# Kernel optimization log

Measured on AMD Instinct MI355X. Metric: run time of the kernel, lower is better.

Reference implementation:

```python
import jax, jax.numpy as jnp
import numpy as np
from jax.ops import segment_sum

NUM_NODES = 100000
HIDDEN = 128
NUM_LAYERS = 3
EDGES = 640000
BN_EPS = 1e-5


def setup_inputs() -> dict:
    key = jax.random.key(0)
    ks = jax.random.split(key, 6)
    edge_index = jax.random.randint(ks[0], (2, EDGES), 0, NUM_NODES, dtype=jnp.int32)
    # xavier-ish init for embedding (hidden-1 dims; last dim is log-degree feature)
    emb_weight = jax.random.normal(ks[1], (NUM_NODES, HIDDEN - 1), dtype=jnp.float32) * 0.02
    # GCNConv linear weights [L, in, out] and biases [L, out]
    Ws = jax.random.normal(ks[2], (NUM_LAYERS, HIDDEN, HIDDEN), dtype=jnp.float32) * (1.0 / np.sqrt(HIDDEN))
    bs = jnp.zeros((NUM_LAYERS, HIDDEN), dtype=jnp.float32)
    gammas = jnp.ones((NUM_LAYERS, HIDDEN), dtype=jnp.float32)
    betas = jnp.zeros((NUM_LAYERS, HIDDEN), dtype=jnp.float32)
    return {"emb_weight": emb_weight, "Ws": Ws, "bs": bs,
            "gammas": gammas, "betas": betas, "edge_index": edge_index}


def reference(emb_weight, Ws, bs, gammas, betas, edge_index):
    row, col = edge_index[0], edge_index[1]  # source, target
    N = emb_weight.shape[0]
    ones_e = jnp.ones(row.shape[0], dtype=emb_weight.dtype)

    # node_degree_features = log(out_degree + 1) (degree of edge_index[0])
    deg_src = segment_sum(ones_e, row, num_segments=N)
    x = jnp.concatenate([emb_weight, jnp.log(deg_src + 1.0)[:, None]], axis=1)  # [N, H]

    # GCN symmetric normalization (add_self_loops=False): deg over targets
    deg = segment_sum(ones_e, col, num_segments=N)
    dinv = jnp.where(deg > 0, jax.lax.rsqrt(jnp.maximum(deg, 1.0)), 0.0)
    norm = dinv[row] * dinv[col]  # [E]

    for i in range(Ws.shape[0]):
        x_prev = x
        h = x @ Ws[i]  # [N, H]
        # scatter-add of normalized messages: out[col] += norm * h[row]
        agg = segment_sum(norm[:, None] * h[row], col, num_segments=N) + bs[i]
        # BatchNorm1d (batch statistics, biased variance)
        mean = agg.mean(axis=0)
        var = agg.var(axis=0)
        x = gammas[i] * (agg - mean) * jax.lax.rsqrt(var + BN_EPS) + betas[i]
        x = jax.nn.relu(x)
        if i > 0:
            x = x + 0.5 * x_prev
    return x
```

## Files before the change

### kernel.cpp

```cpp
#include <hip/hip_runtime.h>
#include <hip/hip_bf16.h>
#include <math.h>

#define BN_EPS 1e-5f

typedef __attribute__((ext_vector_type(8))) short short8v;
typedef __attribute__((ext_vector_type(4))) float f32x4;
typedef __attribute__((ext_vector_type(2))) int int2v;
typedef __attribute__((ext_vector_type(4))) unsigned int uint4v;
typedef __attribute__((ext_vector_type(4))) float float4v;

__device__ inline float bf_lo(unsigned int p) { return __uint_as_float(p << 16); }
__device__ inline float bf_hi(unsigned int p) { return __uint_as_float(p & 0xffff0000u); }
__device__ inline unsigned int packbf(float a, float b) {
    unsigned short lo = __builtin_bit_cast(unsigned short, __float2bfloat16(a));
    unsigned short hi = __builtin_bit_cast(unsigned short, __float2bfloat16(b));
    return (unsigned int)lo | ((unsigned int)hi << 16);
}


__global__ __launch_bounds__(256) void deg_kernel(const int* __restrict__ row, const int* __restrict__ col,
                                                  float* __restrict__ deg_src, float* __restrict__ deg_dst, int E) {
    int e = blockIdx.x * 256 + threadIdx.x;
    if (e < E) {
        atomicAdd(&deg_src[row[e]], 1.0f);
        atomicAdd(&deg_dst[col[e]], 1.0f);
    }
}

__global__ __launch_bounds__(256) void dinv_cnt_kernel(float* __restrict__ deg_dst, int* __restrict__ cnt, int N) {
    int n = blockIdx.x * 256 + threadIdx.x;
    if (n < N) {
        float d = deg_dst[n];
        cnt[n] = (int)d;
        deg_dst[n] = (d > 0.0f) ? rsqrtf(d) : 0.0f;
    }
}

__global__ __launch_bounds__(256) void initx_kernel(const float* __restrict__ emb, const float* __restrict__ deg_src,
                                                    unsigned int* __restrict__ x, int N) {
    int idx = blockIdx.x * 256 + threadIdx.x;
    if (idx < N * 64) {
        int n = idx >> 6, p = idx & 63;
        float v0, v1;
        if (p < 63) {
            v0 = emb[(size_t)n * 127 + 2 * p];
            v1 = emb[(size_t)n * 127 + 2 * p + 1];
        } else {
            v0 = emb[(size_t)n * 127 + 126];
            v1 = logf(deg_src[n] + 1.0f);
        }
        x[idx] = packbf(v0, v1);
    }
}

__global__ __launch_bounds__(256) void wt_kernel(const float* __restrict__ Ws, __hip_bfloat16* __restrict__ Wt) {
    int idx = blockIdx.x * 256 + threadIdx.x;
    if (idx < 3 * 16384) {
        int l = idx >> 14, rem = idx & 16383, c = rem >> 7, k = rem & 127;
        Wt[idx] = __float2bfloat16(Ws[(l << 14) + (k << 7) + c]);
    }
}


__global__ __launch_bounds__(256) void scan_pass1(const int* __restrict__ cnt, int* __restrict__ blockSums,
                                                  int N, int PT) {
    __shared__ int lds[256];
    const int tid = threadIdx.x;
    const int start = (blockIdx.x * 256 + tid) * PT;
    int s = 0;
    for (int i = 0; i < PT; ++i) {
        int idx = start + i;
        if (idx < N) s += cnt[idx];
    }
    lds[tid] = s;
    __syncthreads();
    for (int d = 128; d > 0; d >>= 1) {
        if (tid < d) lds[tid] += lds[tid + d];
        __syncthreads();
    }
    if (tid == 0) blockSums[blockIdx.x] = lds[0];
}

__global__ __launch_bounds__(256) void scan_pass2(const int* __restrict__ blockSums, int* __restrict__ blockOffs) {
    __shared__ int lds[256];
    const int tid = threadIdx.x;
    int v = blockSums[tid];
    lds[tid] = v;
    __syncthreads();
    for (int d = 1; d < 256; d <<= 1) {
        int t = (tid >= d) ? lds[tid - d] : 0;
        __syncthreads();
        lds[tid] += t;
        __syncthreads();
    }
    blockOffs[tid] = lds[tid] - v;
}

__global__ __launch_bounds__(256) void scan_pass3(const int* __restrict__ cnt, const int* __restrict__ blockOffs,
                                                  int* __restrict__ off, int* __restrict__ cur,
                                                  int N, int PT, int E) {
    __shared__ int lds[256];
    const int tid = threadIdx.x;
    const int start = (blockIdx.x * 256 + tid) * PT;
    int s = 0;
    for (int i = 0; i < PT; ++i) {
        int idx = start + i;
        if (idx < N) s += cnt[idx];
    }
    lds[tid] = s;
    __syncthreads();
    for (int d = 1; d < 256; d <<= 1) {
        int t = (tid >= d) ? lds[tid - d] : 0;
        __syncthreads();
        lds[tid] += t;
        __syncthreads();
    }
    int prefix = blockOffs[blockIdx.x] + lds[tid] - s;
    for (int i = 0; i < PT; ++i) {
        int idx = start + i;
        if (idx < N) {
            off[idx] = prefix;
            cur[idx] = prefix;
            prefix += cnt[idx];
        }
    }
    if (blockIdx.x == 0 && tid == 0) off[N] = E;
}

__global__ __launch_bounds__(256) void fill_kernel(const int* __restrict__ row, const int* __restrict__ col,
                                                   const float* __restrict__ dinv, int* __restrict__ cur,
                                                   int2* __restrict__ meta, int E) {
    int e = blockIdx.x * 256 + threadIdx.x;
    if (e < E) {
        int r = row[e], t = col[e];
        int p = atomicAdd(&cur[t], 1);
        meta[p] = make_int2(r, __float_as_int(dinv[r] * dinv[t]));
    }
}


__global__ __launch_bounds__(256) void gemm_mfma(const __hip_bfloat16* __restrict__ X,
                                                 const __hip_bfloat16* __restrict__ Wt,
                                                 __hip_bfloat16* __restrict__ H, float* __restrict__ sums,
                                                 int nStripes, int N) {
    if (blockIdx.x == 0) sums[threadIdx.x] = 0.0f;

    const int lane = threadIdx.x & 63;
    const int wv = threadIdx.x >> 6;
    const int r = lane & 15;
    const int q = lane >> 4;
    const int ch = (blockIdx.x * 4 + wv) & 1;

    short8v bfrag[4][4];
#pragma unroll
    for (int ct = 0; ct < 4; ++ct)
#pragma unroll
        for (int kk = 0; kk < 4; ++kk)
            bfrag[ct][kk] = *(const short8v*)(Wt + ((ch * 64 + ct * 16 + r) << 7) + kk * 32 + q * 8);

    const int totalJobs = nStripes * 2;
    for (int job = blockIdx.x * 4 + wv; job < totalJobs; job += gridDim.x * 4) {
        const int s = job >> 1;
        const int arow = s * 16 + r;
        short8v a0 = {}, a1 = {}, a2 = {}, a3 = {};
        if (arow < N) {
            const __hip_bfloat16* xp = X + ((size_t)arow << 7) + q * 8;
            a0 = *(const short8v*)(xp);
            a1 = *(const short8v*)(xp + 32);
            a2 = *(const short8v*)(xp + 64);
            a3 = *(const short8v*)(xp + 96);
        }
        f32x4 acc[4];
#pragma unroll
        for (int ct = 0; ct < 4; ++ct) {
            f32x4 c = {0.f, 0.f, 0.f, 0.f};
            c = __builtin_amdgcn_mfma_f32_16x16x32_bf16(a0, bfrag[ct][0], c, 0, 0, 0);
            c = __builtin_amdgcn_mfma_f32_16x16x32_bf16(a1, bfrag[ct][1], c, 0, 0, 0);
            c = __builtin_amdgcn_mfma_f32_16x16x32_bf16(a2, bfrag[ct][2], c, 0, 0, 0);
            c = __builtin_amdgcn_mfma_f32_16x16x32_bf16(a3, bfrag[ct][3], c, 0, 0, 0);
            acc[ct] = c;
        }
#pragma unroll
        for (int g = 0; g < 4; ++g) {
            int grow = s * 16 + q * 4 + g;
            if (grow < N) {
                __hip_bfloat16* hp = H + ((size_t)grow << 7) + ch * 64 + r;
#pragma unroll
                for (int ct = 0; ct < 4; ++ct)
                    hp[ct * 16] = __float2bfloat16(acc[ct][g]);
            }
        }
    }
}


__global__ __launch_bounds__(256) void gather_kernel(const __hip_bfloat16* __restrict__ h,
                                                     const int* __restrict__ off, const int2* __restrict__ meta,
                                                     const float* __restrict__ bias,
                                                     unsigned int* __restrict__ aggb, float* __restrict__ sums, int N) {
    __shared__ float sm[2][4][128];
    const int tid = threadIdx.x;
    const int lane = tid & 63;
    const int w = tid >> 6;
    const int g = lane >> 4;
    const int s = lane & 15;

    float b8[8];
    *(float4*)&b8[0] = *(const float4*)&bias[s * 8];
    *(float4*)&b8[4] = *(const float4*)&bias[s * 8 + 4];

    float psum[8], psq[8];
#pragma unroll
    for (int j = 0; j < 8; ++j) { psum[j] = 0.f; psq[j] = 0.f; }

    for (int base = (blockIdx.x * 4 + w) * 2; base < N; base += gridDim.x * 8) {
        const int nA = __builtin_amdgcn_readfirstlane(base);
        const int hasB = (nA + 1 < N);
        const int sA = off[nA];
        const int eA = off[nA + 1];
        const int eB = hasB ? off[nA + 2] : eA;

        float accA[8], accB[8];
#pragma unroll
        for (int j = 0; j < 8; ++j) { accA[j] = 0.f; accB[j] = 0.f; }

        int iA = sA, iB = eA;
        while (iA < eA || iB < eB) {
            int i0A = iA + g, i1A = iA + 4 + g;
            int i0B = iB + g, i1B = iB + 4 + g;
            int idx0A = (i0A < eA) ? i0A : 0;
            int idx1A = (i1A < eA) ? i1A : 0;
            int idx0B = (i0B < eB) ? i0B : 0;
            int idx1B = (i1B < eB) ? i1B : 0;
            int2v m0A = __builtin_nontemporal_load((const int2v*)&meta[idx0A]);
            int2v m1A = __builtin_nontemporal_load((const int2v*)&meta[idx1A]);
            int2v m0B = __builtin_nontemporal_load((const int2v*)&meta[idx0B]);
            int2v m1B = __builtin_nontemporal_load((const int2v*)&meta[idx1B]);
            float w0A = (i0A < eA) ? __int_as_float(m0A[1]) : 0.f;
            float w1A = (i1A < eA) ? __int_as_float(m1A[1]) : 0.f;
            float w0B = (i0B < eB) ? __int_as_float(m0B[1]) : 0.f;
            float w1B = (i1B < eB) ? __int_as_float(m1B[1]) : 0.f;
            short8v h0A = *(const short8v*)(h + ((size_t)m0A[0] << 7) + s * 8);
            short8v h1A = *(const short8v*)(h + ((size_t)m1A[0] << 7) + s * 8);
            short8v h0B = *(const short8v*)(h + ((size_t)m0B[0] << 7) + s * 8);
            short8v h1B = *(const short8v*)(h + ((size_t)m1B[0] << 7) + s * 8);
#pragma unroll
            for (int j = 0; j < 4; ++j) {
                unsigned int u;
                u = ((const unsigned int*)&h0A)[j];
                accA[2 * j]     = fmaf(w0A, bf_lo(u), accA[2 * j]);
                accA[2 * j + 1] = fmaf(w0A, bf_hi(u), accA[2 * j + 1]);
                u = ((const unsigned int*)&h1A)[j];
                accA[2 * j]     = fmaf(w1A, bf_lo(u), accA[2 * j]);
                accA[2 * j + 1] = fmaf(w1A, bf_hi(u), accA[2 * j + 1]);
                u = ((const unsigned int*)&h0B)[j];
                accB[2 * j]     = fmaf(w0B, bf_lo(u), accB[2 * j]);
                accB[2 * j + 1] = fmaf(w0B, bf_hi(u), accB[2 * j + 1]);
                u = ((const unsigned int*)&h1B)[j];
                accB[2 * j]     = fmaf(w1B, bf_lo(u), accB[2 * j]);
                accB[2 * j + 1] = fmaf(w1B, bf_hi(u), accB[2 * j + 1]);
            }
            iA += 8; iB += 8;
        }
#pragma unroll
        for (int j = 0; j < 8; ++j) {
            accA[j] += __shfl_xor(accA[j], 16);
            accA[j] += __shfl_xor(accA[j], 32);
            accA[j] += b8[j];
            accB[j] += __shfl_xor(accB[j], 16);
            accB[j] += __shfl_xor(accB[j], 32);
            accB[j] += b8[j];
        }
        if (g == 0) {
            uint4v pk;
#pragma unroll
            for (int j = 0; j < 4; ++j) pk[j] = packbf(accA[2 * j], accA[2 * j + 1]);
            __builtin_nontemporal_store(pk, (uint4v*)(aggb + ((size_t)nA << 6) + s * 4));
#pragma unroll
            for (int j = 0; j < 8; ++j) {
                psum[j] += accA[j];
                psq[j] = fmaf(accA[j], accA[j], psq[j]);
            }
            if (hasB) {
#pragma unroll
                for (int j = 0; j < 8; ++j) {
                    psum[j] += accB[j];
                    psq[j] = fmaf(accB[j], accB[j], psq[j]);
                }
            }
        } else if (g == 1 && hasB) {
            uint4v pk;
#pragma unroll
            for (int j = 0; j < 4; ++j) pk[j] = packbf(accB[2 * j], accB[2 * j + 1]);
            __builtin_nontemporal_store(pk, (uint4v*)(aggb + ((size_t)(nA + 1) << 6) + s * 4));
        }
    }
    if (g == 0) {
#pragma unroll
        for (int j = 0; j < 8; ++j) {
            sm[0][w][s * 8 + j] = psum[j];
            sm[1][w][s * 8 + j] = psq[j];
        }
    }
    __syncthreads();
    if (tid < 128) {
        atomicAdd(&sums[tid], sm[0][0][tid] + sm[0][1][tid] + sm[0][2][tid] + sm[0][3][tid]);
    } else {
        int c = tid - 128;
        atomicAdd(&sums[128 + c], sm[1][0][c] + sm[1][1][c] + sm[1][2][c] + sm[1][3][c]);
    }
}


template <int MODE>
__global__ __launch_bounds__(256) void bn_apply(const unsigned int* __restrict__ aggb, const float* __restrict__ sums,
                                                const float* __restrict__ gamma, const float* __restrict__ beta,
                                                const uint4* __restrict__ xprev, void* __restrict__ xout,
                                                int NO, float invN) {
    int idx = blockIdx.x * 256 + threadIdx.x;
    if (idx >= NO) return;
    const int c0 = (idx & 15) * 8;

    float su[8], sq[8], gm[8], bt[8];
    *(float4*)&su[0] = *(const float4*)&sums[c0];
    *(float4*)&su[4] = *(const float4*)&sums[c0 + 4];
    *(float4*)&sq[0] = *(const float4*)&sums[128 + c0];
    *(float4*)&sq[4] = *(const float4*)&sums[128 + c0 + 4];
    *(float4*)&gm[0] = *(const float4*)&gamma[c0];
    *(float4*)&gm[4] = *(const float4*)&gamma[c0 + 4];
    *(float4*)&bt[0] = *(const float4*)&beta[c0];
    *(float4*)&bt[4] = *(const float4*)&beta[c0 + 4];

    float sc[8], sh[8];
#pragma unroll
    for (int j = 0; j < 8; ++j) {
        float m = su[j] * invN;
        float v = sq[j] * invN - m * m;
        float inv = rsqrtf(fmaxf(v, 0.0f) + BN_EPS);
        sc[j] = gm[j] * inv;
        sh[j] = bt[j] - m * sc[j];
    }

    uint4v av = __builtin_nontemporal_load((const uint4v*)(aggb + (size_t)idx * 4));
    float r[8];
#pragma unroll
    for (int j = 0; j < 4; ++j) {
        r[2 * j]     = fmaxf(fmaf(bf_lo(av[j]), sc[2 * j],     sh[2 * j]),     0.f);
        r[2 * j + 1] = fmaxf(fmaf(bf_hi(av[j]), sc[2 * j + 1], sh[2 * j + 1]), 0.f);
    }
    if (MODE >= 1) {
        uint4 xv = xprev[idx];
        const unsigned int* xu = (const unsigned int*)&xv;
#pragma unroll
        for (int j = 0; j < 4; ++j) {
            r[2 * j]     = fmaf(0.5f, bf_lo(xu[j]), r[2 * j]);
            r[2 * j + 1] = fmaf(0.5f, bf_hi(xu[j]), r[2 * j + 1]);
        }
    }
    if (MODE == 2) {
        float* op = (float*)xout + (size_t)idx * 8;
        float4v lo = {r[0], r[1], r[2], r[3]};
        float4v hi = {r[4], r[5], r[6], r[7]};
        __builtin_nontemporal_store(lo, (float4v*)op);
        __builtin_nontemporal_store(hi, (float4v*)(op + 4));
    } else {
        unsigned int pk[4];
#pragma unroll
        for (int j = 0; j < 4; ++j) pk[j] = packbf(r[2 * j], r[2 * j + 1]);
        ((uint4*)xout)[idx] = *(uint4*)pk;
    }
}


extern "C" void kernel_launch(void* const* d_in, const int* in_sizes, int n_in,
                              void* d_out, int out_size, void* d_ws, size_t ws_size,
                              hipStream_t stream) {
    const float* emb    = (const float*)d_in[0];
    const float* Ws     = (const float*)d_in[1];
    const float* bs     = (const float*)d_in[2];
    const float* gammas = (const float*)d_in[3];
    const float* betas  = (const float*)d_in[4];
    const int*   ei     = (const int*)d_in[5];

    const int N = in_sizes[0] / 127;
    const int E = in_sizes[5] / 2;
    const int* row = ei;
    const int* col = ei + E;
    float* out = (float*)d_out;

    const size_t NH = (size_t)N * 128;
    __hip_bfloat16* XA = (__hip_bfloat16*)d_ws;
    __hip_bfloat16* XB = XA + NH;
    unsigned int*  AGG = (unsigned int*)(XB + NH);
    int2*         meta = (int2*)(AGG + NH / 2);
    __hip_bfloat16* Wt = (__hip_bfloat16*)(meta + E);
    float* deg_src = (float*)(Wt + 3 * 16384);
    float* dinvb   = deg_src + N;
    float* sums    = dinvb + N;
    int*   cnt     = (int*)(sums + 256);
    int*   cur     = cnt + N;
    int*   blockSums = cur + N;
    int*   blockOffs = blockSums + 256;
    int*   off     = blockOffs + 256;

    const int NO = (int)(NH / 8);
    const int PT = (N + 65535) / 65536;
    const int nStripes = (N + 15) / 16;
    const float invN = 1.0f / (float)N;

    hipMemsetAsync(deg_src, 0, sizeof(float) * 2 * (size_t)N, stream);
    wt_kernel<<<(3 * 16384 + 255) / 256, 256, 0, stream>>>(Ws, Wt);
    deg_kernel<<<(E + 255) / 256, 256, 0, stream>>>(row, col, deg_src, dinvb, E);
    dinv_cnt_kernel<<<(N + 255) / 256, 256, 0, stream>>>(dinvb, cnt, N);
    initx_kernel<<<(N * 64 + 255) / 256, 256, 0, stream>>>(emb, deg_src, (unsigned int*)XA, N);
    scan_pass1<<<256, 256, 0, stream>>>(cnt, blockSums, N, PT);
    scan_pass2<<<1, 256, 0, stream>>>(blockSums, blockOffs);
    scan_pass3<<<256, 256, 0, stream>>>(cnt, blockOffs, off, cur, N, PT, E);
    fill_kernel<<<(E + 255) / 256, 256, 0, stream>>>(row, col, dinvb, cur, meta, E);

    const __hip_bfloat16* xin[3]  = {XA, XA, XB};
    __hip_bfloat16*       hbuf[3] = {XB, XB, XA};

    for (int i = 0; i < 3; ++i) {
        gemm_mfma<<<1024, 256, 0, stream>>>(xin[i], Wt + (size_t)i * 16384, hbuf[i], sums, nStripes, N);
        gather_kernel<<<2048, 256, 0, stream>>>(hbuf[i], off, meta, bs + i * 128, AGG, sums, N);
        if (i == 0)
            bn_apply<0><<<(NO + 255) / 256, 256, 0, stream>>>(AGG, sums, gammas, betas,
                                                              (const uint4*)xin[i], (void*)XA, NO, invN);
        else if (i == 1)
            bn_apply<1><<<(NO + 255) / 256, 256, 0, stream>>>(AGG, sums, gammas + 128, betas + 128,
                                                              (const uint4*)xin[i], (void*)XB, NO, invN);
        else
            bn_apply<2><<<(NO + 255) / 256, 256, 0, stream>>>(AGG, sums, gammas + 256, betas + 256,
                                                              (const uint4*)xin[i], (void*)out, NO, invN);
    }
}
```

Baseline: 459.0 us.

## Fuse BatchNorm apply into next layer's MFMA GEMM prologue

BatchNorm normalization, ReLU and the residual add of layers 0 and 1 now run inside the next layer's GEMM, which builds its A fragments from the normalized values. One of the two column-half waves also writes the new activation for the later residual. This removes two standalone bn_apply launches and one round trip of the activation through memory. The cost is that the BN scale and shift are recomputed per fragment. The output buffer serves as scratch for the last H, and the BN sums now alternate between two buffers, with each fused kernel zeroing the next layer's sums.

```diff
diff --git a/kernel.cpp b/kernel.cpp
--- a/kernel.cpp
+++ b/kernel.cpp
@@ -179,6 +179,105 @@
             c = __builtin_amdgcn_mfma_f32_16x16x32_bf16(a1, bfrag[ct][1], c, 0, 0, 0);
             c = __builtin_amdgcn_mfma_f32_16x16x32_bf16(a2, bfrag[ct][2], c, 0, 0, 0);
             c = __builtin_amdgcn_mfma_f32_16x16x32_bf16(a3, bfrag[ct][3], c, 0, 0, 0);
+            acc[ct] = c;
+        }
+#pragma unroll
+        for (int g = 0; g < 4; ++g) {
+            int grow = s * 16 + q * 4 + g;
+            if (grow < N) {
+                __hip_bfloat16* hp = H + ((size_t)grow << 7) + ch * 64 + r;
+#pragma unroll
+                for (int ct = 0; ct < 4; ++ct)
+                    hp[ct * 16] = __float2bfloat16(acc[ct][g]);
+            }
+        }
+    }
+}
+
+
+template <int MODE>
+__global__ __launch_bounds__(256) void bn_gemm(const unsigned int* __restrict__ aggb, const float* __restrict__ sums,
+                                               const float* __restrict__ gamma, const float* __restrict__ beta,
+                                               const unsigned int* __restrict__ xprevb, unsigned int* __restrict__ xoutb,
+                                               const __hip_bfloat16* __restrict__ Wt, __hip_bfloat16* __restrict__ H,
+                                               float* __restrict__ sumsNext, int nStripes, int N, float invN) {
+    if (blockIdx.x == 0) sumsNext[threadIdx.x] = 0.0f;
+
+    const int lane = threadIdx.x & 63;
+    const int wv = threadIdx.x >> 6;
+    const int r = lane & 15;
+    const int q = lane >> 4;
+    const int ch = (blockIdx.x * 4 + wv) & 1;
+
+    short8v bfrag[4][4];
+#pragma unroll
+    for (int ct = 0; ct < 4; ++ct)
+#pragma unroll
+        for (int kk = 0; kk < 4; ++kk)
+            bfrag[ct][kk] = *(const short8v*)(Wt + ((ch * 64 + ct * 16 + r) << 7) + kk * 32 + q * 8);
+
+    const int totalJobs = nStripes * 2;
+    for (int job = blockIdx.x * 4 + wv; job < totalJobs; job += gridDim.x * 4) {
+        const int s = job >> 1;
+        const int arow = s * 16 + r;
+        short8v a[4] = {{}, {}, {}, {}};
+        if (arow < N) {
+            const size_t rbase = ((size_t)arow << 6) + q * 4;
+#pragma unroll
+            for (int kk = 0; kk < 4; ++kk) {
+                const int c0 = q * 8 + kk * 32;
+                float su[8], sq[8], gm[8], bt[8];
+                *(float4*)&su[0] = *(const float4*)&sums[c0];
+                *(float4*)&su[4] = *(const float4*)&sums[c0 + 4];
+                *(float4*)&sq[0] = *(const float4*)&sums[128 + c0];
+                *(float4*)&sq[4] = *(const float4*)&sums[128 + c0 + 4];
+                *(float4*)&gm[0] = *(const float4*)&gamma[c0];
+                *(float4*)&gm[4] = *(const float4*)&gamma[c0 + 4];
+                *(float4*)&bt[0] = *(const float4*)&beta[c0];
+                *(float4*)&bt[4] = *(const float4*)&beta[c0 + 4];
+                float sc[8], sh[8];
+#pragma unroll
+                for (int j = 0; j < 8; ++j) {
+                    float m = su[j] * invN;
+                    float v = sq[j] * invN - m * m;
+                    float inv = rsqrtf(fmaxf(v, 0.0f) + BN_EPS);
+                    sc[j] = gm[j] * inv;
+                    sh[j] = bt[j] - m * sc[j];
+                }
+                uint4 av = *(const uint4*)(aggb + rbase + kk * 16);
+                const unsigned int* au = (const unsigned int*)&av;
+                float x[8];
+#pragma unroll
+                for (int j = 0; j < 4; ++j) {
+                    x[2 * j]     = fmaxf(fmaf(bf_lo(au[j]), sc[2 * j],     sh[2 * j]),     0.f);
+                    x[2 * j + 1] = fmaxf(fmaf(bf_hi(au[j]), sc[2 * j + 1], sh[2 * j + 1]), 0.f);
+                }
+                if (MODE == 1) {
+                    uint4 xv = *(const uint4*)(xprevb + rbase + kk * 16);
+                    const unsigned int* xu = (const unsigned int*)&xv;
+#pragma unroll
+                    for (int j = 0; j < 4; ++j) {
+                        x[2 * j]     = fmaf(0.5f, bf_lo(xu[j]), x[2 * j]);
+                        x[2 * j + 1] = fmaf(0.5f, bf_hi(xu[j]), x[2 * j + 1]);
+                    }
+                }
+                uint4 pk;
+                unsigned int* pku = (unsigned int*)&pk;
+#pragma unroll
+                for (int j = 0; j < 4; ++j) pku[j] = packbf(x[2 * j], x[2 * j + 1]);
+                if (ch == 0) *(uint4*)(xoutb + rbase + kk * 16) = pk;
+#pragma unroll
+                for (int j = 0; j < 4; ++j) ((unsigned int*)&a[kk])[j] = pku[j];
+            }
+        }
+        f32x4 acc[4];
+#pragma unroll
+        for (int ct = 0; ct < 4; ++ct) {
+            f32x4 c = {0.f, 0.f, 0.f, 0.f};
+            c = __builtin_amdgcn_mfma_f32_16x16x32_bf16(a[0], bfrag[ct][0], c, 0, 0, 0);
+            c = __builtin_amdgcn_mfma_f32_16x16x32_bf16(a[1], bfrag[ct][1], c, 0, 0, 0);
+            c = __builtin_amdgcn_mfma_f32_16x16x32_bf16(a[2], bfrag[ct][2], c, 0, 0, 0);
+            c = __builtin_amdgcn_mfma_f32_16x16x32_bf16(a[3], bfrag[ct][3], c, 0, 0, 0);
             acc[ct] = c;
         }
 #pragma unroll
@@ -313,11 +412,10 @@
 }
 
 
-template <int MODE>
-__global__ __launch_bounds__(256) void bn_apply(const unsigned int* __restrict__ aggb, const float* __restrict__ sums,
-                                                const float* __restrict__ gamma, const float* __restrict__ beta,
-                                                const uint4* __restrict__ xprev, void* __restrict__ xout,
-                                                int NO, float invN) {
+__global__ __launch_bounds__(256) void bn_out(const unsigned int* __restrict__ aggb, const float* __restrict__ sums,
+                                              const float* __restrict__ gamma, const float* __restrict__ beta,
+                                              const uint4* __restrict__ xprev, float* __restrict__ xout,
+                                              int NO, float invN) {
     int idx = blockIdx.x * 256 + threadIdx.x;
     if (idx >= NO) return;
     const int c0 = (idx & 15) * 8;
@@ -349,27 +447,18 @@
         r[2 * j]     = fmaxf(fmaf(bf_lo(av[j]), sc[2 * j],     sh[2 * j]),     0.f);
         r[2 * j + 1] = fmaxf(fmaf(bf_hi(av[j]), sc[2 * j + 1], sh[2 * j + 1]), 0.f);
     }
-    if (MODE >= 1) {
-        uint4 xv = xprev[idx];
-        const unsigned int* xu = (const unsigned int*)&xv;
-#pragma unroll
-        for (int j = 0; j < 4; ++j) {
-            r[2 * j]     = fmaf(0.5f, bf_lo(xu[j]), r[2 * j]);
-            r[2 * j + 1] = fmaf(0.5f, bf_hi(xu[j]), r[2 * j + 1]);
-        }
-    }
-    if (MODE == 2) {
-        float* op = (float*)xout + (size_t)idx * 8;
-        float4v lo = {r[0], r[1], r[2], r[3]};
-        float4v hi = {r[4], r[5], r[6], r[7]};
-        __builtin_nontemporal_store(lo, (float4v*)op);
-        __builtin_nontemporal_store(hi, (float4v*)(op + 4));
-    } else {
-        unsigned int pk[4];
-#pragma unroll
-        for (int j = 0; j < 4; ++j) pk[j] = packbf(r[2 * j], r[2 * j + 1]);
-        ((uint4*)xout)[idx] = *(uint4*)pk;
-    }
+    uint4 xv = xprev[idx];
+    const unsigned int* xu = (const unsigned int*)&xv;
+#pragma unroll
+    for (int j = 0; j < 4; ++j) {
+        r[2 * j]     = fmaf(0.5f, bf_lo(xu[j]), r[2 * j]);
+        r[2 * j + 1] = fmaf(0.5f, bf_hi(xu[j]), r[2 * j + 1]);
+    }
+    float* op = xout + (size_t)idx * 8;
+    float4v lo = {r[0], r[1], r[2], r[3]};
+    float4v hi = {r[4], r[5], r[6], r[7]};
+    __builtin_nontemporal_store(lo, (float4v*)op);
+    __builtin_nontemporal_store(hi, (float4v*)(op + 4));
 }
 
 
@@ -397,12 +486,15 @@
     __hip_bfloat16* Wt = (__hip_bfloat16*)(meta + E);
     float* deg_src = (float*)(Wt + 3 * 16384);
     float* dinvb   = deg_src + N;
-    float* sums    = dinvb + N;
-    int*   cnt     = (int*)(sums + 256);
+    float* sumsA   = dinvb + N;
+    float* sumsB   = sumsA + 256;
+    int*   cnt     = (int*)(sumsB + 256);
     int*   cur     = cnt + N;
     int*   blockSums = cur + N;
     int*   blockOffs = blockSums + 256;
     int*   off     = blockOffs + 256;
+
+    __hip_bfloat16* H2 = (__hip_bfloat16*)out;
 
     const int NO = (int)(NH / 8);
     const int PT = (N + 65535) / 65536;
@@ -419,20 +511,17 @@
     scan_pass3<<<256, 256, 0, stream>>>(cnt, blockOffs, off, cur, N, PT, E);
     fill_kernel<<<(E + 255) / 256, 256, 0, stream>>>(row, col, dinvb, cur, meta, E);
 
-    const __hip_bfloat16* xin[3]  = {XA, XA, XB};
-    __hip_bfloat16*       hbuf[3] = {XB, XB, XA};
-
-    for (int i = 0; i < 3; ++i) {
-        gemm_mfma<<<1024, 256, 0, stream>>>(xin[i], Wt + (size_t)i * 16384, hbuf[i], sums, nStripes, N);
-        gather_kernel<<<2048, 256, 0, stream>>>(hbuf[i], off, meta, bs + i * 128, AGG, sums, N);
-        if (i == 0)
-            bn_apply<0><<<(NO + 255) / 256, 256, 0, stream>>>(AGG, sums, gammas, betas,
-                                                              (const uint4*)xin[i], (void*)XA, NO, invN);
-        else if (i == 1)
-            bn_apply<1><<<(NO + 255) / 256, 256, 0, stream>>>(AGG, sums, gammas + 128, betas + 128,
-                                                              (const uint4*)xin[i], (void*)XB, NO, invN);
-        else
-            bn_apply<2><<<(NO + 255) / 256, 256, 0, stream>>>(AGG, sums, gammas + 256, betas + 256,
-                                                              (const uint4*)xin[i], (void*)out, NO, invN);
-    }
-}
+    gemm_mfma<<<1024, 256, 0, stream>>>(XA, Wt, XB, sumsA, nStripes, N);
+    gather_kernel<<<2048, 256, 0, stream>>>(XB, off, meta, bs, AGG, sumsA, N);
+
+    bn_gemm<0><<<1024, 256, 0, stream>>>(AGG, sumsA, gammas, betas, nullptr,
+                                         (unsigned int*)XA, Wt + 16384, XB, sumsB, nStripes, N, invN);
+    gather_kernel<<<2048, 256, 0, stream>>>(XB, off, meta, bs + 128, AGG, sumsB, N);
+
+    bn_gemm<1><<<1024, 256, 0, stream>>>(AGG, sumsB, gammas + 128, betas + 128, (const unsigned int*)XA,
+                                         (unsigned int*)XB, Wt + 2 * 16384, H2, sumsA, nStripes, N, invN);
+    gather_kernel<<<2048, 256, 0, stream>>>(H2, off, meta, bs + 256, AGG, sumsA, N);
+
+    bn_out<<<(NO + 255) / 256, 256, 0, stream>>>(AGG, sumsA, gammas + 256, betas + 256,
+                                                 (const uint4*)XB, out, NO, invN);
+}
```

Result: slower. 496.3 us (+8.1%).
